# Kernel optimization log

Hardware: AMD Instinct MI355X
Metric: run time of the kernel (lower is better)

Reference implementation:

```python
import jax, jax.numpy as jnp
import numpy as np

TEMPERATURE = 8.0


def setup_inputs() -> dict:
    key = jax.random.key(0)
    kq, kk, kv, kc = jax.random.split(key, 4)
    B, L, D = 4, 4096, 64
    q = jax.random.normal(kq, (B, L, D), dtype=jnp.float32)
    k = jax.random.normal(kk, (B, L, D), dtype=jnp.float32)
    v = jax.random.normal(kv, (B, L, D), dtype=jnp.float32)
    # vectors = stack(softmax(randn(d_v)), softmax(randn(d_v)))  (dim=0 softmax over d_v)
    raw = jax.random.normal(kc, (2, D), dtype=jnp.float32)
    vectors = jax.nn.softmax(raw, axis=1)
    return {"q": q, "k": k, "v": v, "vectors": vectors}


def reference(q, k, v, vectors):
    # Original builds diagonal core tensors cores[t,t,t] = vectors[.,t] for t < min(dimen, len_q),
    # then einsum('pqk,bip,bjq,bkr->bijr') and sums over j. With a diagonal core this collapses to:
    #   out[b,i,r] = sum_{t<m} q[b,i,t] * w[t] * ksum[b,t] * v[b,t,r]
    # where w = 0.5*(c1+c2)/temperature and ksum[b,t] = sum_j k[b,j,t].
    B, L, D = q.shape
    m = min(D, L)  # static python int
    w = 0.5 * (vectors[0, :m] + vectors[1, :m]) / TEMPERATURE          # [m]
    ksum = jnp.sum(k[:, :, :m], axis=1)                                 # [B, m]
    coef = w[None, :] * ksum                                            # [B, m]
    output = jnp.einsum('bit,bt,btr->bir', q[:, :, :m], coef, v[:, :m, :])  # [B, L, D]
    attn = jnp.einsum('bid,bjd->bij', q, k)                             # [B, L, L]
    return (output, attn)
```

## Files before the change

### kernel.cpp

```cpp
#include <hip/hip_runtime.h>
#include <stdint.h>

#define BB 4
#define LL 4096
#define DD 64

typedef __attribute__((ext_vector_type(8))) short bf16x8;
typedef __attribute__((ext_vector_type(4))) float f32x4;

static __device__ __forceinline__ unsigned short f2bf(float x) {
    unsigned int u = __builtin_bit_cast(unsigned int, x);
    u += 0x7fffu + ((u >> 16) & 1u);
    return (unsigned short)(u >> 16);
}

__global__ __launch_bounds__(256) void convert_kernel(
    const float* __restrict__ q, const float* __restrict__ k,
    unsigned short* __restrict__ qbf, unsigned short* __restrict__ kbf,
    float* __restrict__ part)
{
    const int NBQ = (BB * LL * DD) / 2048;
    int bid = blockIdx.x;
    bool is_k = bid >= NBQ;
    const float* src = is_k ? k : q;
    unsigned short* dst = is_k ? kbf : qbf;
    int cb = is_k ? (bid - NBQ) : bid;
    int tid = threadIdx.x;

    size_t idx0 = (size_t)cb * 2048 + (size_t)tid * 8;
    float4 f0 = *(const float4*)(src + idx0);
    float4 f1 = *(const float4*)(src + idx0 + 4);
    float f[8] = {f0.x, f0.y, f0.z, f0.w, f1.x, f1.y, f1.z, f1.w};

    unsigned short u[8];
    #pragma unroll
    for (int e = 0; e < 8; e++) u[e] = f2bf(f[e]);
    uint4 pk;
    pk.x = (unsigned)u[0] | ((unsigned)u[1] << 16);
    pk.y = (unsigned)u[2] | ((unsigned)u[3] << 16);
    pk.z = (unsigned)u[4] | ((unsigned)u[5] << 16);
    pk.w = (unsigned)u[6] | ((unsigned)u[7] << 16);
    *(uint4*)(dst + idx0) = pk;

    if (is_k) {
        __shared__ float red[256][8];
        #pragma unroll
        for (int e = 0; e < 8; e++) red[tid][e] = f[e];
        __syncthreads();
        if (tid < 64) {
            int g = tid >> 3, e = tid & 7;
            float s = 0.f;
            #pragma unroll
            for (int r = 0; r < 32; r++) s += red[r * 8 + g][e];
            part[(size_t)cb * 64 + tid] = s;
        }
    }
}

__global__ __launch_bounds__(256) void out_kernel(
    const float* __restrict__ q, const float* __restrict__ v,
    const float* __restrict__ vec, const float* __restrict__ part,
    float* __restrict__ out)
{
    __shared__ float csh[64];
    __shared__ float Vl[64][65];
    __shared__ float qs[32][65];

    int bid = blockIdx.x;
    int b   = bid >> 7;
    int i0  = (bid & 127) << 5;
    int tid = threadIdx.x;

    if (tid < 64) {
        const float* pp = part + (size_t)b * 128 * 64 + tid;
        float s = 0.f;
        #pragma unroll 8
        for (int c = 0; c < 128; c++) s += pp[c * 64];
        csh[tid] = 0.0625f * (vec[tid] + vec[64 + tid]) * s;
    }
    {
        const float* vb = v + (size_t)b * LL * DD;
        #pragma unroll
        for (int it = 0; it < 4; it++) {
            int idx4 = it * 256 + tid;
            int t  = idx4 >> 4;
            int r4 = (idx4 & 15) << 2;
            float4 w = *(const float4*)(vb + (size_t)idx4 * 4);
            Vl[t][r4 + 0] = w.x; Vl[t][r4 + 1] = w.y;
            Vl[t][r4 + 2] = w.z; Vl[t][r4 + 3] = w.w;
        }
    }
    __syncthreads();
    {
        const float* qb = q + (size_t)b * LL * DD;
        int row = tid >> 3;
        int t0  = (tid & 7) << 3;
        const float* src = qb + (size_t)(i0 + row) * DD + t0;
        float4 a0 = *(const float4*)(src);
        float4 a1 = *(const float4*)(src + 4);
        float fa[8] = {a0.x,a0.y,a0.z,a0.w,a1.x,a1.y,a1.z,a1.w};
        #pragma unroll
        for (int e = 0; e < 8; e++) qs[row][t0 + e] = fa[e] * csh[t0 + e];
    }
    __syncthreads();

    int ii = tid >> 3;
    int g  = tid & 7;
    float acc[8] = {0,0,0,0,0,0,0,0};
    #pragma unroll 8
    for (int t = 0; t < 64; t++) {
        float qv = qs[ii][t];
        #pragma unroll
        for (int j = 0; j < 8; j++) acc[j] += qv * Vl[t][g * 8 + j];
    }
    float* op = out + (size_t)b * LL * DD + (size_t)(i0 + ii) * DD + g * 8;
    float4 s0 = {acc[0], acc[1], acc[2], acc[3]};
    float4 s1 = {acc[4], acc[5], acc[6], acc[7]};
    *(float4*)(op)     = s0;
    *(float4*)(op + 4) = s1;
}

__global__ __launch_bounds__(512, 4) void attn_kernel(
    const unsigned short* __restrict__ qbf,
    const unsigned short* __restrict__ kbf,
    float* __restrict__ attn)
{
    int bid = blockIdx.x;
    int swz = (bid & 7) * 64 + (bid >> 3);
    int b   = swz >> 7;
    int ti  = swz & 127;
    int i0  = ti * 32;

    int tid  = threadIdx.x;
    int w    = tid >> 6;
    int lane = tid & 63;
    int lr = lane & 15;
    int g  = lane >> 4;
    int lk = g * 8;
    int jb = g * 4;

    const unsigned short* qb = qbf + (size_t)b * LL * DD;
    const unsigned short* kb = kbf + (size_t)b * LL * DD;
    float* ab = attn + (size_t)b * LL * LL;

    bf16x8 qf[2][2];
    #pragma unroll
    for (int m = 0; m < 2; m++)
        #pragma unroll
        for (int kk = 0; kk < 2; kk++)
            qf[m][kk] = *(const bf16x8*)(
                qb + (size_t)(i0 + m * 16 + lr) * DD + kk * 32 + lk);

    #pragma unroll
    for (int tj = 0; tj < 8; tj++) {
        int j0 = tj * 512 + w * 64;

        bf16x8 kf[4][2];
        #pragma unroll
        for (int n = 0; n < 4; n++)
            #pragma unroll
            for (int kk = 0; kk < 2; kk++)
                kf[n][kk] = *(const bf16x8*)(
                    kb + (size_t)(j0 + n * 16 + lr) * DD + kk * 32 + lk);

        f32x4 acc[2][4];
        #pragma unroll
        for (int m = 0; m < 2; m++)
            #pragma unroll
            for (int n = 0; n < 4; n++)
                acc[m][n] = (f32x4){0.f, 0.f, 0.f, 0.f};

        #pragma unroll
        for (int kk = 0; kk < 2; kk++)
            #pragma unroll
            for (int m = 0; m < 2; m++)
                #pragma unroll
                for (int n = 0; n < 4; n++)
                    acc[m][n] = __builtin_amdgcn_mfma_f32_16x16x32_bf16(
                        kf[n][kk], qf[m][kk], acc[m][n], 0, 0, 0);

        #pragma unroll
        for (int m = 0; m < 2; m++) {
            size_t roff = (size_t)(i0 + m * 16 + lr) * LL;
            #pragma unroll
            for (int n = 0; n < 4; n++)
                *(f32x4*)(ab + roff + j0 + n * 16 + jb) = acc[m][n];
        }
    }
}

extern "C" void kernel_launch(void* const* d_in, const int* in_sizes, int n_in,
                              void* d_out, int out_size, void* d_ws, size_t ws_size,
                              hipStream_t stream) {
    const float* q   = (const float*)d_in[0];
    const float* k   = (const float*)d_in[1];
    const float* v   = (const float*)d_in[2];
    const float* vec = (const float*)d_in[3];

    float* out  = (float*)d_out;
    float* attn = out + (size_t)BB * LL * DD;

    unsigned short* qbf = (unsigned short*)d_ws;
    unsigned short* kbf = qbf + (size_t)BB * LL * DD;
    float* part = (float*)(kbf + (size_t)BB * LL * DD);

    convert_kernel<<<1024, 256, 0, stream>>>(q, k, qbf, kbf, part);
    out_kernel<<<512, 256, 0, stream>>>(q, v, vec, part, out);
    attn_kernel<<<512, 512, 0, stream>>>(qbf, kbf, attn);
}
```

Baseline: 78.31 us.

## Software-pipeline K fragment loads and split attn tiles across more blocks

The attention kernel now prefetches K fragments two iterations ahead in a triple-buffered register array, with a sched_barrier so global loads overlap the MFMA work and the output stores. The grid is changed from 512 blocks of 512 threads to 1024 blocks of 256 threads, each covering half of the j range, and the block swizzle is updated to match. The aim is to hide load latency and improve scheduling across CUs. The cost is higher register pressure from the extra K and accumulator buffers, and the launch-bounds occupancy hint has been dropped.

```diff
diff --git a/kernel.cpp b/kernel.cpp
--- a/kernel.cpp
+++ b/kernel.cpp
@@ -120,16 +120,56 @@
     *(float4*)(op + 4) = s1;
 }
 
-__global__ __launch_bounds__(512, 4) void attn_kernel(
+#define LOADK(buf, t) do {                                                    \
+    int j0_ = jbase + (t) * 256 + w * 64;                                     \
+    const unsigned short* kp_ = kb + (size_t)(j0_ + lr) * DD + lk;            \
+    _Pragma("unroll")                                                         \
+    for (int n_ = 0; n_ < 4; n_++)                                            \
+      _Pragma("unroll")                                                       \
+      for (int kk_ = 0; kk_ < 2; kk_++)                                       \
+        kf[buf][n_][kk_] = *(const bf16x8*)(kp_ + (size_t)n_ * 16 * DD + kk_ * 32); \
+} while (0)
+
+#define DOMFMA(abuf, kbuf) do {                                               \
+    _Pragma("unroll")                                                         \
+    for (int m_ = 0; m_ < 2; m_++)                                            \
+      _Pragma("unroll")                                                       \
+      for (int n_ = 0; n_ < 4; n_++)                                          \
+        acc[abuf][m_][n_] = (f32x4){0.f, 0.f, 0.f, 0.f};                      \
+    _Pragma("unroll")                                                         \
+    for (int kk_ = 0; kk_ < 2; kk_++)                                         \
+      _Pragma("unroll")                                                       \
+      for (int m_ = 0; m_ < 2; m_++)                                          \
+        _Pragma("unroll")                                                     \
+        for (int n_ = 0; n_ < 4; n_++)                                        \
+          acc[abuf][m_][n_] = __builtin_amdgcn_mfma_f32_16x16x32_bf16(        \
+              kf[kbuf][n_][kk_], qf[m_][kk_], acc[abuf][m_][n_], 0, 0, 0);    \
+} while (0)
+
+#define STOREC(abuf, t) do {                                                  \
+    int j0_ = jbase + (t) * 256 + w * 64;                                     \
+    _Pragma("unroll")                                                         \
+    for (int m_ = 0; m_ < 2; m_++) {                                          \
+      float* p_ = ab + (size_t)(i0 + m_ * 16 + lr) * LL + j0_ + jb;           \
+      _Pragma("unroll")                                                       \
+      for (int n_ = 0; n_ < 4; n_++)                                          \
+        *(f32x4*)(p_ + n_ * 16) = acc[abuf][m_][n_];                          \
+    }                                                                         \
+} while (0)
+
+__global__ __launch_bounds__(256) void attn_kernel(
     const unsigned short* __restrict__ qbf,
     const unsigned short* __restrict__ kbf,
     float* __restrict__ attn)
 {
     int bid = blockIdx.x;
-    int swz = (bid & 7) * 64 + (bid >> 3);
-    int b   = swz >> 7;
-    int ti  = swz & 127;
+    int swz = (bid & 7) * 128 + (bid >> 3);
+    int b   = swz >> 8;
+    int rem = swz & 255;
+    int ti  = rem >> 1;
+    int jh  = rem & 1;
     int i0  = ti * 32;
+    int jbase = jh * 2048;
 
     int tid  = threadIdx.x;
     int w    = tid >> 6;
@@ -151,41 +191,18 @@
             qf[m][kk] = *(const bf16x8*)(
                 qb + (size_t)(i0 + m * 16 + lr) * DD + kk * 32 + lk);
 
+    bf16x8 kf[3][4][2];
+    f32x4 acc[2][2][4];
+
+    LOADK(0, 0);
+    LOADK(1, 1);
+
     #pragma unroll
-    for (int tj = 0; tj < 8; tj++) {
-        int j0 = tj * 512 + w * 64;
-
-        bf16x8 kf[4][2];
-        #pragma unroll
-        for (int n = 0; n < 4; n++)
-            #pragma unroll
-            for (int kk = 0; kk < 2; kk++)
-                kf[n][kk] = *(const bf16x8*)(
-                    kb + (size_t)(j0 + n * 16 + lr) * DD + kk * 32 + lk);
-
-        f32x4 acc[2][4];
-        #pragma unroll
-        for (int m = 0; m < 2; m++)
-            #pragma unroll
-            for (int n = 0; n < 4; n++)
-                acc[m][n] = (f32x4){0.f, 0.f, 0.f, 0.f};
-
-        #pragma unroll
-        for (int kk = 0; kk < 2; kk++)
-            #pragma unroll
-            for (int m = 0; m < 2; m++)
-                #pragma unroll
-                for (int n = 0; n < 4; n++)
-                    acc[m][n] = __builtin_amdgcn_mfma_f32_16x16x32_bf16(
-                        kf[n][kk], qf[m][kk], acc[m][n], 0, 0, 0);
-
-        #pragma unroll
-        for (int m = 0; m < 2; m++) {
-            size_t roff = (size_t)(i0 + m * 16 + lr) * LL;
-            #pragma unroll
-            for (int n = 0; n < 4; n++)
-                *(f32x4*)(ab + roff + j0 + n * 16 + jb) = acc[m][n];
-        }
+    for (int t = 0; t < 8; ++t) {
+        if (t < 6) LOADK((t + 2) % 3, t + 2);
+        __builtin_amdgcn_sched_barrier(0);
+        DOMFMA(t & 1, t % 3);
+        STOREC(t & 1, t);
     }
 }
 
@@ -206,5 +223,5 @@
 
     convert_kernel<<<1024, 256, 0, stream>>>(q, k, qbf, kbf, part);
     out_kernel<<<512, 256, 0, stream>>>(q, v, vec, part, out);
-    attn_kernel<<<512, 512, 0, stream>>>(qbf, kbf, attn);
-}
+    attn_kernel<<<1024, 256, 0, stream>>>(qbf, kbf, attn);
+}
```

Result: no change. 79.63 us (+1.7%).
